# Kernel optimization log

Hardware: AMD Instinct MI355X
Metric: run time of the kernel (lower is better)

Reference implementation:

```python
import jax, jax.numpy as jnp
import numpy as np

N_NODES = 50000
N_EDGES = 640000
IN_CH = 32
OUT_CH = 64
H1 = 2 * IN_CH   # 64
H2 = 4 * IN_CH   # 128


def _sage_conv(x, src, dst, w_l, b_l, w_r, n_nodes):
    """PyG SAGEConv (mean aggr): out = mean_{j in N(i)} x_j @ w_l + b_l + x_i @ w_r."""
    msg = x[src]                                                  # [E, d] gather
    agg = jax.ops.segment_sum(msg, dst, num_segments=n_nodes)    # [N, d]
    cnt = jax.ops.segment_sum(jnp.ones_like(dst, x.dtype), dst, num_segments=n_nodes)
    mean = agg / jnp.maximum(cnt, 1.0)[:, None]                   # empty neighborhoods -> 0
    return mean @ w_l + b_l + x @ w_r


def setup_inputs() -> dict:
    key = jax.random.key(0)
    ks = jax.random.split(key, 9)
    x = jax.random.normal(ks[0], (N_NODES, IN_CH), dtype=jnp.float32)
    edge_index = jax.random.randint(ks[1], (2, N_EDGES), 0, N_NODES, dtype=jnp.int32)

    def glorot(k, shape):
        fan_in, fan_out = shape
        s = jnp.sqrt(6.0 / (fan_in + fan_out))
        return jax.random.uniform(k, shape, jnp.float32, -s, s)

    return {
        "x": x,
        "edge_index": edge_index,
        "w1_l": glorot(ks[2], (IN_CH, H1)), "b1": jnp.zeros((H1,), jnp.float32),
        "w1_r": glorot(ks[3], (IN_CH, H1)),
        "w2_l": glorot(ks[4], (H1, H2)), "b2": jnp.zeros((H2,), jnp.float32),
        "w2_r": glorot(ks[5], (H1, H2)),
        "w3_l": glorot(ks[6], (H2, OUT_CH)), "b3": jnp.zeros((OUT_CH,), jnp.float32),
        "w3_r": glorot(ks[7], (H2, OUT_CH)),
    }


def reference(x, edge_index, w1_l, b1, w1_r, w2_l, b2, w2_r, w3_l, b3, w3_r):
    n = x.shape[0]
    src, dst = edge_index[0], edge_index[1]
    h = jax.nn.relu(_sage_conv(x, src, dst, w1_l, b1, w1_r, n))
    h = jax.nn.relu(_sage_conv(h, src, dst, w2_l, b2, w2_r, n))
    return _sage_conv(h, src, dst, w3_l, b3, w3_r, n)
```

## Files before the change

### kernel.cpp

```cpp
#include <hip/hip_runtime.h>


typedef short bf8 __attribute__((ext_vector_type(8)));
typedef float f32x4 __attribute__((ext_vector_type(4)));

__device__ inline ushort bf16rn(float f) {
    unsigned u = __float_as_uint(f);
    return (ushort)((u + 0x7FFFu + ((u >> 16) & 1u)) >> 16);
}
__device__ inline float bf16tof(ushort h) {
    return __uint_as_float(((unsigned)h) << 16);
}
__device__ inline void split8(const float4 pa, const float4 pb, bf8& hi, bf8& lo) {
    const float v[8] = {pa.x, pa.y, pa.z, pa.w, pb.x, pb.y, pb.z, pb.w};
#pragma unroll
    for (int j = 0; j < 8; ++j) {
        const ushort h = bf16rn(v[j]);
        hi[j] = (short)h;
        lo[j] = (short)bf16rn(v[j] - bf16tof(h));
    }
}

__global__ __launch_bounds__(256) void prep_kernel(
    const float* __restrict__ x,
    const float* __restrict__ w1l, const float* __restrict__ w1r,
    const float* __restrict__ w2l, const float* __restrict__ w2r,
    const float* __restrict__ w3l, const float* __restrict__ w3r,
    ushort* __restrict__ wprep, int* __restrict__ cnt,
    ushort* __restrict__ xh, int nN, int nCntZero)
{
    const int g = blockIdx.x * 256 + threadIdx.x;
    const int n = gridDim.x * 256;
    for (int f = g; f < 9216; f += n) {
        int base, KCs, oc0, d0, wstride;
        const float *wa, *wb;
        if (f < 1024)      { base = 0;    KCs = 2; oc0 = 0;  wa = w1l; wb = w1r; d0 = 32;  wstride = 64;  }
        else if (f < 3072) { base = 1024; KCs = 4; oc0 = 0;  wa = w2l; wb = w2r; d0 = 64;  wstride = 128; }
        else if (f < 5120) { base = 3072; KCs = 4; oc0 = 64; wa = w2l; wb = w2r; d0 = 64;  wstride = 128; }
        else if (f < 7168) { base = 5120; KCs = 4; oc0 = 0;  wa = w3l; wb = w3l; d0 = 128; wstride = 64;  }
        else               { base = 7168; KCs = 4; oc0 = 0;  wa = w3r; wb = w3r; d0 = 128; wstride = 64;  }
        const int local = f - base;
        const int lane = local & 63;
        const int s = (local >> 6) & 1;
        const int kcct = local >> 7;
        const int kc = kcct % KCs;
        const int ct = kcct / KCs;
        const int col = oc0 + ct * 16 + (lane & 15);
        const int k0 = kc * 32 + (lane >> 4) * 8;
        ushort h8[8];
#pragma unroll
        for (int j = 0; j < 8; ++j) {
            const int k = k0 + j;
            const float* wr = (k < d0) ? (wa + (size_t)k * wstride)
                                       : (wb + (size_t)(k - d0) * wstride);
            const float v = wr[col];
            const ushort h = bf16rn(v);
            h8[j] = (s == 0) ? h : bf16rn(v - bf16tof(h));
        }
        *reinterpret_cast<int4*>(wprep + (size_t)f * 8) = *reinterpret_cast<const int4*>(h8);
    }
    for (int i = g; i < nCntZero / 4; i += n)
        reinterpret_cast<int4*>(cnt)[i] = make_int4(0, 0, 0, 0);
    const int nxv = nN * 4;
    for (int i = g; i < nxv; i += n) {
        const float4 a = reinterpret_cast<const float4*>(x)[i * 2 + 0];
        const float4 b = reinterpret_cast<const float4*>(x)[i * 2 + 1];
        const float v[8] = {a.x, a.y, a.z, a.w, b.x, b.y, b.z, b.w};
        bf8 h;
#pragma unroll
        for (int j = 0; j < 8; ++j) h[j] = (short)bf16rn(v[j]);
        reinterpret_cast<bf8*>(xh)[i] = h;
    }
}

__global__ __launch_bounds__(256) void count_kernel(const int* __restrict__ dst,
                                                    int* __restrict__ cnt,
                                                    ushort* __restrict__ pos, int nE) {
    int i = blockIdx.x * blockDim.x + threadIdx.x;
    int e0 = i * 4;
    if (e0 + 3 < nE) {
        int4 d = *reinterpret_cast<const int4*>(dst + e0);
        ushort4 p;
        p.x = (ushort)atomicAdd(&cnt[d.x], 1);
        p.y = (ushort)atomicAdd(&cnt[d.y], 1);
        p.z = (ushort)atomicAdd(&cnt[d.z], 1);
        p.w = (ushort)atomicAdd(&cnt[d.w], 1);
        *reinterpret_cast<ushort4*>(pos + e0) = p;
    } else {
        for (int e = e0; e < nE; ++e) pos[e] = (ushort)atomicAdd(&cnt[dst[e]], 1);
    }
}

__global__ __launch_bounds__(256) void scan_blocks(const int* __restrict__ cnt,
                                                   int* __restrict__ rowptr,
                                                   int* __restrict__ partials, int nN) {
    __shared__ int wsum[4];
    const int t = threadIdx.x;
    const int lane = t & 63, wid = t >> 6;
    const int base = blockIdx.x * 1024 + t * 4;

    int4 v = make_int4(0, 0, 0, 0);
    if (base + 3 < nN) {
        v = *reinterpret_cast<const int4*>(cnt + base);
    } else {
        if (base + 0 < nN) v.x = cnt[base + 0];
        if (base + 1 < nN) v.y = cnt[base + 1];
        if (base + 2 < nN) v.z = cnt[base + 2];
        if (base + 3 < nN) v.w = cnt[base + 3];
    }
    const int s = v.x + v.y + v.z + v.w;

    int inc = s;
#pragma unroll
    for (int d = 1; d < 64; d <<= 1) {
        int u = __shfl_up(inc, d);
        if (lane >= d) inc += u;
    }
    if (lane == 63) wsum[wid] = inc;
    __syncthreads();
    int woff = 0;
#pragma unroll
    for (int w = 0; w < 4; ++w) woff += (w < wid) ? wsum[w] : 0;

    const int excl = woff + inc - s;
    int4 o;
    o.x = excl; o.y = excl + v.x; o.z = excl + v.x + v.y; o.w = excl + v.x + v.y + v.z;
    if (base + 3 < nN) {
        *reinterpret_cast<int4*>(rowptr + base) = o;
    } else {
        if (base + 0 < nN) rowptr[base + 0] = o.x;
        if (base + 1 < nN) rowptr[base + 1] = o.y;
        if (base + 2 < nN) rowptr[base + 2] = o.z;
        if (base + 3 < nN) rowptr[base + 3] = o.w;
    }
    if (t == 255) partials[blockIdx.x] = woff + inc;
}

__global__ __launch_bounds__(256) void scan_add(int* __restrict__ rowptr,
                                                const int* __restrict__ partials,
                                                int nN, int nE) {
    __shared__ int soff;
    const int t = threadIdx.x;
    if (t < 64) {
        int v = (t < blockIdx.x) ? partials[t] : 0;
#pragma unroll
        for (int d = 32; d >= 1; d >>= 1) v += __shfl_xor(v, d);
        if (t == 0) soff = v;
    }
    __syncthreads();
    const int off = soff;
    const int base = blockIdx.x * 1024 + t * 4;
    if (base + 3 < nN) {
        int4 v = *reinterpret_cast<int4*>(rowptr + base);
        v.x += off; v.y += off; v.z += off; v.w += off;
        *reinterpret_cast<int4*>(rowptr + base) = v;
    } else {
        if (base + 0 < nN) rowptr[base + 0] += off;
        if (base + 1 < nN) rowptr[base + 1] += off;
        if (base + 2 < nN) rowptr[base + 2] += off;
        if (base + 3 < nN) rowptr[base + 3] += off;
    }
    if (blockIdx.x == 0 && t == 0) rowptr[nN] = nE;
}

__global__ __launch_bounds__(256) void fill_kernel(const int* __restrict__ src,
                                                   const int* __restrict__ dst,
                                                   const ushort* __restrict__ pos,
                                                   const int* __restrict__ rowptr,
                                                   ushort* __restrict__ csr_src, int nE) {
    int i = blockIdx.x * blockDim.x + threadIdx.x;
    int e0 = i * 4;
    if (e0 + 3 < nE) {
        int4 s4 = *reinterpret_cast<const int4*>(src + e0);
        int4 d4 = *reinterpret_cast<const int4*>(dst + e0);
        ushort4 p4 = *reinterpret_cast<const ushort4*>(pos + e0);
        csr_src[rowptr[d4.x] + p4.x] = (ushort)s4.x;
        csr_src[rowptr[d4.y] + p4.y] = (ushort)s4.y;
        csr_src[rowptr[d4.z] + p4.z] = (ushort)s4.z;
        csr_src[rowptr[d4.w] + p4.w] = (ushort)s4.w;
    } else {
        for (int e = e0; e < nE; ++e)
            csr_src[rowptr[dst[e]] + pos[e]] = (ushort)src[e];
    }
}

__global__ __launch_bounds__(256) void fused_layer1(
    const float* __restrict__ x, const ushort* __restrict__ xh,
    const int* __restrict__ rowptr, const ushort* __restrict__ csr_src,
    const ushort* __restrict__ wfrag, const float* __restrict__ b1,
    ushort* __restrict__ h1h, ushort* __restrict__ h1l, int nN)
{
    __shared__ float tile[64 * 36];
    __shared__ ushort wlds[1024 * 8];

    const int tid = threadIdx.x;
    const int node0 = blockIdx.x * 64;

    {
        const int4* wsrc = reinterpret_cast<const int4*>(wfrag);
        int4* wl = reinterpret_cast<int4*>(wlds);
        for (int i = tid; i < 1024; i += 256) wl[i] = wsrc[i];
    }
    {
        const int nl = tid >> 2;
        const int c = tid & 3;
        const int node = node0 + nl;
        float acc[8] = {0.f, 0.f, 0.f, 0.f, 0.f, 0.f, 0.f, 0.f};
        if (node < nN) {
            const int beg = rowptr[node], end = rowptr[node + 1];
            int e = beg;
            for (; e + 7 < end; e += 8) {
                int si[8];
#pragma unroll
                for (int j = 0; j < 8; ++j) si[j] = csr_src[e + j];
                bf8 v[8];
#pragma unroll
                for (int j = 0; j < 8; ++j)
                    v[j] = *reinterpret_cast<const bf8*>(xh + (size_t)si[j] * 32 + c * 8);
#pragma unroll
                for (int k = 0; k < 8; ++k)
#pragma unroll
                    for (int j = 0; j < 8; ++j) acc[k] += bf16tof((ushort)v[j][k]);
            }
            for (; e < end; ++e) {
                bf8 v = *reinterpret_cast<const bf8*>(xh + (size_t)csr_src[e] * 32 + c * 8);
#pragma unroll
                for (int k = 0; k < 8; ++k) acc[k] += bf16tof((ushort)v[k]);
            }
            const float sc = 1.0f / (float)max(end - beg, 1);
#pragma unroll
            for (int k = 0; k < 8; ++k) acc[k] *= sc;
        }
        *reinterpret_cast<float4*>(&tile[nl * 36 + c * 8 + 0]) =
            make_float4(acc[0], acc[1], acc[2], acc[3]);
        *reinterpret_cast<float4*>(&tile[nl * 36 + c * 8 + 4]) =
            make_float4(acc[4], acc[5], acc[6], acc[7]);
    }
    __syncthreads();

    const int w = tid >> 6, lane = tid & 63;
    const int rloc = w * 16 + (lane & 15);
    const int arow = min(node0 + rloc, nN - 1);
    const int kg = lane >> 4;
    bf8 ahi[2], alo[2];
    {
        const float* tp = &tile[rloc * 36 + kg * 8];
        split8(*reinterpret_cast<const float4*>(tp),
               *reinterpret_cast<const float4*>(tp + 4), ahi[0], alo[0]);
    }
    {
        const float* rp = x + (size_t)arow * 32 + kg * 8;
        split8(*reinterpret_cast<const float4*>(rp),
               *reinterpret_cast<const float4*>(rp + 4), ahi[1], alo[1]);
    }
    const bf8* bgl = reinterpret_cast<const bf8*>(wlds);
#pragma unroll
    for (int ct = 0; ct < 4; ++ct) {
        f32x4 acc = {0.f, 0.f, 0.f, 0.f};
#pragma unroll
        for (int kc = 0; kc < 2; ++kc) {
            const bf8 bhi = bgl[((ct * 2 + kc) * 2 + 0) * 64 + lane];
            const bf8 blo = bgl[((ct * 2 + kc) * 2 + 1) * 64 + lane];
            acc = __builtin_amdgcn_mfma_f32_16x16x32_bf16(ahi[kc], bhi, acc, 0, 0, 0);
            acc = __builtin_amdgcn_mfma_f32_16x16x32_bf16(ahi[kc], blo, acc, 0, 0, 0);
            acc = __builtin_amdgcn_mfma_f32_16x16x32_bf16(alo[kc], bhi, acc, 0, 0, 0);
        }
        const int col = ct * 16 + (lane & 15);
        const float bv = b1[col];
#pragma unroll
        for (int r = 0; r < 4; ++r) {
            const int node = node0 + w * 16 + (lane >> 4) * 4 + r;
            if (node < nN) {
                const float o = fmaxf(acc[r] + bv, 0.f);
                const ushort hi = bf16rn(o);
                h1h[(size_t)node * 64 + col] = hi;
                h1l[(size_t)node * 64 + col] = bf16rn(o - bf16tof(hi));
            }
        }
    }
}

__global__ __launch_bounds__(256) void fused_layer2(
    const ushort* __restrict__ h1h, const ushort* __restrict__ h1l,
    const int* __restrict__ rowptr, const ushort* __restrict__ csr_src,
    const ushort* __restrict__ wfrag, const float* __restrict__ b2,
    ushort* __restrict__ h2h, ushort* __restrict__ h2l, int nN)
{
    __shared__ float tile[64 * 68];

    const int tid = threadIdx.x;
    const int node0 = blockIdx.x * 64;

    {
        const int c = tid & 7;
        const int nl0 = tid >> 3;
#pragma unroll
        for (int p = 0; p < 2; ++p) {
            const int nl = p * 32 + nl0;
            const int node = node0 + nl;
            float acc[8] = {0.f, 0.f, 0.f, 0.f, 0.f, 0.f, 0.f, 0.f};
            if (node < nN) {
                const int beg = rowptr[node], end = rowptr[node + 1];
                int e = beg;
                for (; e + 7 < end; e += 8) {
                    int si[8];
#pragma unroll
                    for (int j = 0; j < 8; ++j) si[j] = csr_src[e + j];
                    bf8 v[8];
#pragma unroll
                    for (int j = 0; j < 8; ++j)
                        v[j] = *reinterpret_cast<const bf8*>(h1h + (size_t)si[j] * 64 + c * 8);
#pragma unroll
                    for (int k = 0; k < 8; ++k)
#pragma unroll
                        for (int j = 0; j < 8; ++j) acc[k] += bf16tof((ushort)v[j][k]);
                }
                for (; e < end; ++e) {
                    bf8 v = *reinterpret_cast<const bf8*>(h1h + (size_t)csr_src[e] * 64 + c * 8);
#pragma unroll
                    for (int k = 0; k < 8; ++k) acc[k] += bf16tof((ushort)v[k]);
                }
                const float sc = 1.0f / (float)max(end - beg, 1);
#pragma unroll
                for (int k = 0; k < 8; ++k) acc[k] *= sc;
            }
            *reinterpret_cast<float4*>(&tile[nl * 68 + c * 8 + 0]) =
                make_float4(acc[0], acc[1], acc[2], acc[3]);
            *reinterpret_cast<float4*>(&tile[nl * 68 + c * 8 + 4]) =
                make_float4(acc[4], acc[5], acc[6], acc[7]);
        }
    }
    __syncthreads();

    const int w = tid >> 6, lane = tid & 63;
    const int rloc = w * 16 + (lane & 15);
    const int arow = min(node0 + rloc, nN - 1);
    const int kg = lane >> 4;
    bf8 ahi[4], alo[4];
#pragma unroll
    for (int kc = 0; kc < 2; ++kc) {
        const float* tp = &tile[rloc * 68 + kc * 32 + kg * 8];
        split8(*reinterpret_cast<const float4*>(tp),
               *reinterpret_cast<const float4*>(tp + 4), ahi[kc], alo[kc]);
    }
#pragma unroll
    for (int kc = 2; kc < 4; ++kc) {
        const size_t off = (size_t)arow * 64 + (kc - 2) * 32 + kg * 8;
        ahi[kc] = *reinterpret_cast<const bf8*>(h1h + off);
        alo[kc] = *reinterpret_cast<const bf8*>(h1l + off);
    }
#pragma unroll
    for (int ct = 0; ct < 8; ++ct) {
        const int sec = ct >> 2, ctl = ct & 3;
        const bf8* bgl = reinterpret_cast<const bf8*>(wfrag) + sec * 2048;
        f32x4 acc = {0.f, 0.f, 0.f, 0.f};
#pragma unroll
        for (int kc = 0; kc < 4; ++kc) {
            const bf8 bhi = bgl[((ctl * 4 + kc) * 2 + 0) * 64 + lane];
            const bf8 blo = bgl[((ctl * 4 + kc) * 2 + 1) * 64 + lane];
            acc = __builtin_amdgcn_mfma_f32_16x16x32_bf16(ahi[kc], bhi, acc, 0, 0, 0);
            acc = __builtin_amdgcn_mfma_f32_16x16x32_bf16(ahi[kc], blo, acc, 0, 0, 0);
            acc = __builtin_amdgcn_mfma_f32_16x16x32_bf16(alo[kc], bhi, acc, 0, 0, 0);
        }
        const int col = ct * 16 + (lane & 15);
        const float bv = b2[col];
#pragma unroll
        for (int r = 0; r < 4; ++r) {
            const int node = node0 + w * 16 + (lane >> 4) * 4 + r;
            if (node < nN) {
                const float o = fmaxf(acc[r] + bv, 0.f);
                const ushort hi = bf16rn(o);
                h2h[(size_t)node * 128 + col] = hi;
                h2l[(size_t)node * 128 + col] = bf16rn(o - bf16tof(hi));
            }
        }
    }
}

__global__ __launch_bounds__(256) void mfma_dual(
    const ushort* __restrict__ h2h, const ushort* __restrict__ h2l,
    const ushort* __restrict__ wfrag, const float* __restrict__ b3,
    ushort* __restrict__ t3h, float* __restrict__ r3, int nN)
{
    const int tid = threadIdx.x;
    const int w = tid >> 6, lane = tid & 63;
    const int node0 = blockIdx.x * 64;
    const int arow = min(node0 + w * 16 + (lane & 15), nN - 1);
    const int kg = lane >> 4;

    bf8 ahi[4], alo[4];
#pragma unroll
    for (int kc = 0; kc < 4; ++kc) {
        const size_t off = (size_t)arow * 128 + kc * 32 + kg * 8;
        ahi[kc] = *reinterpret_cast<const bf8*>(h2h + off);
        alo[kc] = *reinterpret_cast<const bf8*>(h2l + off);
    }
#pragma unroll
    for (int sel = 0; sel < 2; ++sel) {
        const bf8* bgl = reinterpret_cast<const bf8*>(wfrag) + sel * 2048;
#pragma unroll
        for (int ct = 0; ct < 4; ++ct) {
            f32x4 acc = {0.f, 0.f, 0.f, 0.f};
#pragma unroll
            for (int kc = 0; kc < 4; ++kc) {
                const bf8 bhi = bgl[((ct * 4 + kc) * 2 + 0) * 64 + lane];
                const bf8 blo = bgl[((ct * 4 + kc) * 2 + 1) * 64 + lane];
                acc = __builtin_amdgcn_mfma_f32_16x16x32_bf16(ahi[kc], bhi, acc, 0, 0, 0);
                acc = __builtin_amdgcn_mfma_f32_16x16x32_bf16(ahi[kc], blo, acc, 0, 0, 0);
                acc = __builtin_amdgcn_mfma_f32_16x16x32_bf16(alo[kc], bhi, acc, 0, 0, 0);
            }
            const int col = ct * 16 + (lane & 15);
#pragma unroll
            for (int r = 0; r < 4; ++r) {
                const int node = node0 + w * 16 + (lane >> 4) * 4 + r;
                if (node < nN) {
                    if (sel) r3[(size_t)node * 64 + col] = acc[r] + b3[col];
                    else     t3h[(size_t)node * 64 + col] = bf16rn(acc[r]);
                }
            }
        }
    }
}

__global__ __launch_bounds__(256) void final_gather(
    const ushort* __restrict__ t3h, const int* __restrict__ rowptr,
    const ushort* __restrict__ csr_src, const float* __restrict__ r3,
    float* __restrict__ dout, int nN)
{
    const int tid = threadIdx.x;
    const int node = blockIdx.x * 32 + (tid >> 3);
    const int c = tid & 7;
    if (node >= nN) return;
    const int beg = rowptr[node], end = rowptr[node + 1];
    float acc[8] = {0.f, 0.f, 0.f, 0.f, 0.f, 0.f, 0.f, 0.f};
    int e = beg;
    for (; e + 7 < end; e += 8) {
        int si[8];
#pragma unroll
        for (int j = 0; j < 8; ++j) si[j] = csr_src[e + j];
        bf8 v[8];
#pragma unroll
        for (int j = 0; j < 8; ++j)
            v[j] = *reinterpret_cast<const bf8*>(t3h + (size_t)si[j] * 64 + c * 8);
#pragma unroll
        for (int k = 0; k < 8; ++k)
#pragma unroll
            for (int j = 0; j < 8; ++j) acc[k] += bf16tof((ushort)v[j][k]);
    }
    for (; e < end; ++e) {
        bf8 v = *reinterpret_cast<const bf8*>(t3h + (size_t)csr_src[e] * 64 + c * 8);
#pragma unroll
        for (int k = 0; k < 8; ++k) acc[k] += bf16tof((ushort)v[k]);
    }
    const float sc = 1.0f / (float)max(end - beg, 1);
    const float4 a0 = reinterpret_cast<const float4*>(r3)[(size_t)node * 16 + c * 2 + 0];
    const float4 a1 = reinterpret_cast<const float4*>(r3)[(size_t)node * 16 + c * 2 + 1];
    float4 o0, o1;
    o0.x = fmaf(acc[0], sc, a0.x); o0.y = fmaf(acc[1], sc, a0.y);
    o0.z = fmaf(acc[2], sc, a0.z); o0.w = fmaf(acc[3], sc, a0.w);
    o1.x = fmaf(acc[4], sc, a1.x); o1.y = fmaf(acc[5], sc, a1.y);
    o1.z = fmaf(acc[6], sc, a1.z); o1.w = fmaf(acc[7], sc, a1.w);
    reinterpret_cast<float4*>(dout)[(size_t)node * 16 + c * 2 + 0] = o0;
    reinterpret_cast<float4*>(dout)[(size_t)node * 16 + c * 2 + 1] = o1;
}

extern "C" void kernel_launch(void* const* d_in, const int* in_sizes, int n_in,
                              void* d_out, int out_size, void* d_ws, size_t ws_size,
                              hipStream_t stream) {
    const float* x   = (const float*)d_in[0];
    const int*   ei  = (const int*)d_in[1];
    const float* w1l = (const float*)d_in[2];
    const float* b1  = (const float*)d_in[3];
    const float* w1r = (const float*)d_in[4];
    const float* w2l = (const float*)d_in[5];
    const float* b2  = (const float*)d_in[6];
    const float* w2r = (const float*)d_in[7];
    const float* w3l = (const float*)d_in[8];
    const float* b3  = (const float*)d_in[9];
    const float* w3r = (const float*)d_in[10];

    const int nN = in_sizes[0] / 32;
    const int nE = in_sizes[1] / 2;
    const int* src = ei;
    const int* dst = ei + nE;
    const int nB = (nN + 1023) / 1024;
    const int nCntZero = (nN + 63) & ~63;

    char* ws = (char*)d_ws;
    size_t o = 0;
    auto alloc = [&](size_t nbytes) {
        char* p = ws + o;
        o += (nbytes + 255) & ~(size_t)255;
        return p;
    };
    int*    cnt      = (int*)alloc((size_t)nCntZero * sizeof(int));
    ushort* pos      = (ushort*)alloc((size_t)nE * sizeof(ushort));
    int*    partials = (int*)alloc(64 * sizeof(int));
    int*    rowptr   = (int*)alloc(((size_t)nN + 1) * sizeof(int));
    ushort* csr_src  = (ushort*)alloc((size_t)nE * sizeof(ushort));
    ushort* wprep    = (ushort*)alloc((size_t)9216 * 8 * sizeof(ushort));
    ushort* xh       = (ushort*)alloc((size_t)nN * 32 * sizeof(ushort));
    ushort* h1h      = (ushort*)alloc((size_t)nN * 64 * sizeof(ushort));
    ushort* h1l      = (ushort*)alloc((size_t)nN * 64 * sizeof(ushort));
    ushort* h2h      = (ushort*)alloc((size_t)nN * 128 * sizeof(ushort));
    ushort* h2l      = (ushort*)alloc((size_t)nN * 128 * sizeof(ushort));
    ushort* t3h      = (ushort*)alloc((size_t)nN * 64 * sizeof(ushort));
    float*  r3       = (float*)alloc((size_t)nN * 64 * sizeof(float));

    prep_kernel<<<784, 256, 0, stream>>>(x, w1l, w1r, w2l, w2r, w3l, w3r,
                                         wprep, cnt, xh, nN, nCntZero);
    count_kernel<<<(nE / 4 + 255) / 256, 256, 0, stream>>>(dst, cnt, pos, nE);
    scan_blocks<<<nB, 256, 0, stream>>>(cnt, rowptr, partials, nN);
    scan_add<<<nB, 256, 0, stream>>>(rowptr, partials, nN, nE);
    fill_kernel<<<(nE / 4 + 255) / 256, 256, 0, stream>>>(src, dst, pos, rowptr, csr_src, nE);

    const int xblk = (nN + 63) / 64;

    fused_layer1<<<xblk, 256, 0, stream>>>(x, xh, rowptr, csr_src, wprep, b1, h1h, h1l, nN);
    fused_layer2<<<xblk, 256, 0, stream>>>(h1h, h1l, rowptr, csr_src,
                                           wprep + (size_t)1024 * 8, b2, h2h, h2l, nN);
    mfma_dual<<<xblk, 256, 0, stream>>>(h2h, h2l, wprep + (size_t)5120 * 8, b3, t3h, r3, nN);
    final_gather<<<(nN + 31) / 32, 256, 0, stream>>>(t3h, rowptr, csr_src, r3, (float*)d_out, nN);
}
```

Before: 141.1 us.

## Halve node tile in fused layers, split MFMA columns across waves, store r3 as bf16

Layers 1 and 2 now handle 32 nodes per 256-thread block instead of 64. Each gathering thread covers a narrower feature slice (4 channels in layer 1), and in the MFMA phase the four waves split into two row groups and two column groups. Layer 1 reads weight fragments directly from global memory instead of staging them in LDS. Together this doubles the block count and cuts per-thread serial gather work. Separately, the layer-3 root term r3 is stored as bf16 instead of fp32, halving that intermediate's traffic at the cost of some output precision.

```diff
diff --git a/kernel.cpp b/kernel.cpp
--- a/kernel.cpp
+++ b/kernel.cpp
@@ -2,6 +2,7 @@
 
 
 typedef short bf8 __attribute__((ext_vector_type(8)));
+typedef short bf4 __attribute__((ext_vector_type(4)));
 typedef float f32x4 __attribute__((ext_vector_type(4)));
 
 __device__ inline ushort bf16rn(float f) {
@@ -190,20 +191,104 @@
     const ushort* __restrict__ wfrag, const float* __restrict__ b1,
     ushort* __restrict__ h1h, ushort* __restrict__ h1l, int nN)
 {
-    __shared__ float tile[64 * 36];
-    __shared__ ushort wlds[1024 * 8];
+    __shared__ float tile[32 * 36];
 
     const int tid = threadIdx.x;
-    const int node0 = blockIdx.x * 64;
+    const int node0 = blockIdx.x * 32;
 
     {
-        const int4* wsrc = reinterpret_cast<const int4*>(wfrag);
-        int4* wl = reinterpret_cast<int4*>(wlds);
-        for (int i = tid; i < 1024; i += 256) wl[i] = wsrc[i];
-    }
+        const int nl = tid >> 3;
+        const int c = tid & 7;
+        const int node = node0 + nl;
+        float acc[4] = {0.f, 0.f, 0.f, 0.f};
+        if (node < nN) {
+            const int beg = rowptr[node], end = rowptr[node + 1];
+            int e = beg;
+            for (; e + 7 < end; e += 8) {
+                int si[8];
+#pragma unroll
+                for (int j = 0; j < 8; ++j) si[j] = csr_src[e + j];
+                bf4 v[8];
+#pragma unroll
+                for (int j = 0; j < 8; ++j)
+                    v[j] = *reinterpret_cast<const bf4*>(xh + (size_t)si[j] * 32 + c * 4);
+#pragma unroll
+                for (int k = 0; k < 4; ++k)
+#pragma unroll
+                    for (int j = 0; j < 8; ++j) acc[k] += bf16tof((ushort)v[j][k]);
+            }
+            for (; e < end; ++e) {
+                bf4 v = *reinterpret_cast<const bf4*>(xh + (size_t)csr_src[e] * 32 + c * 4);
+#pragma unroll
+                for (int k = 0; k < 4; ++k) acc[k] += bf16tof((ushort)v[k]);
+            }
+            const float sc = 1.0f / (float)max(end - beg, 1);
+#pragma unroll
+            for (int k = 0; k < 4; ++k) acc[k] *= sc;
+        }
+        *reinterpret_cast<float4*>(&tile[nl * 36 + c * 4]) =
+            make_float4(acc[0], acc[1], acc[2], acc[3]);
+    }
+    __syncthreads();
+
+    const int w = tid >> 6, lane = tid & 63;
+    const int rg = w & 1, cg = w >> 1;
+    const int rloc = rg * 16 + (lane & 15);
+    const int arow = min(node0 + rloc, nN - 1);
+    const int kg = lane >> 4;
+    bf8 ahi[2], alo[2];
     {
-        const int nl = tid >> 2;
-        const int c = tid & 3;
+        const float* tp = &tile[rloc * 36 + kg * 8];
+        split8(*reinterpret_cast<const float4*>(tp),
+               *reinterpret_cast<const float4*>(tp + 4), ahi[0], alo[0]);
+    }
+    {
+        const float* rp = x + (size_t)arow * 32 + kg * 8;
+        split8(*reinterpret_cast<const float4*>(rp),
+               *reinterpret_cast<const float4*>(rp + 4), ahi[1], alo[1]);
+    }
+    const bf8* bgl = reinterpret_cast<const bf8*>(wfrag);
+#pragma unroll
+    for (int cc = 0; cc < 2; ++cc) {
+        const int ct = cg * 2 + cc;
+        f32x4 acc = {0.f, 0.f, 0.f, 0.f};
+#pragma unroll
+        for (int kc = 0; kc < 2; ++kc) {
+            const bf8 bhi = bgl[((ct * 2 + kc) * 2 + 0) * 64 + lane];
+            const bf8 blo = bgl[((ct * 2 + kc) * 2 + 1) * 64 + lane];
+            acc = __builtin_amdgcn_mfma_f32_16x16x32_bf16(ahi[kc], bhi, acc, 0, 0, 0);
+            acc = __builtin_amdgcn_mfma_f32_16x16x32_bf16(ahi[kc], blo, acc, 0, 0, 0);
+            acc = __builtin_amdgcn_mfma_f32_16x16x32_bf16(alo[kc], bhi, acc, 0, 0, 0);
+        }
+        const int col = ct * 16 + (lane & 15);
+        const float bv = b1[col];
+#pragma unroll
+        for (int r = 0; r < 4; ++r) {
+            const int node = node0 + rg * 16 + (lane >> 4) * 4 + r;
+            if (node < nN) {
+                const float o = fmaxf(acc[r] + bv, 0.f);
+                const ushort hi = bf16rn(o);
+                h1h[(size_t)node * 64 + col] = hi;
+                h1l[(size_t)node * 64 + col] = bf16rn(o - bf16tof(hi));
+            }
+        }
+    }
+}
+
+__global__ __launch_bounds__(256) void fused_layer2(
+    const ushort* __restrict__ h1h, const ushort* __restrict__ h1l,
+    const int* __restrict__ rowptr, const ushort* __restrict__ csr_src,
+    const ushort* __restrict__ wfrag, const float* __restrict__ b2,
+    ushort* __restrict__ h2h, ushort* __restrict__ h2l, int nN)
+{
+    __shared__ float tile[32 * 68];
+
+    const int tid = threadIdx.x;
+    const int node0 = blockIdx.x * 32;
+
+    {
+        const int nl = tid >> 3;
+        const int c = tid & 7;
         const int node = node0 + nl;
         float acc[8] = {0.f, 0.f, 0.f, 0.f, 0.f, 0.f, 0.f, 0.f};
         if (node < nN) {
@@ -216,14 +301,14 @@
                 bf8 v[8];
 #pragma unroll
                 for (int j = 0; j < 8; ++j)
-                    v[j] = *reinterpret_cast<const bf8*>(xh + (size_t)si[j] * 32 + c * 8);
+                    v[j] = *reinterpret_cast<const bf8*>(h1h + (size_t)si[j] * 64 + c * 8);
 #pragma unroll
                 for (int k = 0; k < 8; ++k)
 #pragma unroll
                     for (int j = 0; j < 8; ++j) acc[k] += bf16tof((ushort)v[j][k]);
             }
             for (; e < end; ++e) {
-                bf8 v = *reinterpret_cast<const bf8*>(xh + (size_t)csr_src[e] * 32 + c * 8);
+                bf8 v = *reinterpret_cast<const bf8*>(h1h + (size_t)csr_src[e] * 64 + c * 8);
 #pragma unroll
                 for (int k = 0; k < 8; ++k) acc[k] += bf16tof((ushort)v[k]);
             }
@@ -231,109 +316,16 @@
 #pragma unroll
             for (int k = 0; k < 8; ++k) acc[k] *= sc;
         }
-        *reinterpret_cast<float4*>(&tile[nl * 36 + c * 8 + 0]) =
+        *reinterpret_cast<float4*>(&tile[nl * 68 + c * 8 + 0]) =
             make_float4(acc[0], acc[1], acc[2], acc[3]);
-        *reinterpret_cast<float4*>(&tile[nl * 36 + c * 8 + 4]) =
+        *reinterpret_cast<float4*>(&tile[nl * 68 + c * 8 + 4]) =
             make_float4(acc[4], acc[5], acc[6], acc[7]);
     }
     __syncthreads();
 
     const int w = tid >> 6, lane = tid & 63;
-    const int rloc = w * 16 + (lane & 15);
-    const int arow = min(node0 + rloc, nN - 1);
-    const int kg = lane >> 4;
-    bf8 ahi[2], alo[2];
-    {
-        const float* tp = &tile[rloc * 36 + kg * 8];
-        split8(*reinterpret_cast<const float4*>(tp),
-               *reinterpret_cast<const float4*>(tp + 4), ahi[0], alo[0]);
-    }
-    {
-        const float* rp = x + (size_t)arow * 32 + kg * 8;
-        split8(*reinterpret_cast<const float4*>(rp),
-               *reinterpret_cast<const float4*>(rp + 4), ahi[1], alo[1]);
-    }
-    const bf8* bgl = reinterpret_cast<const bf8*>(wlds);
-#pragma unroll
-    for (int ct = 0; ct < 4; ++ct) {
-        f32x4 acc = {0.f, 0.f, 0.f, 0.f};
-#pragma unroll
-        for (int kc = 0; kc < 2; ++kc) {
-            const bf8 bhi = bgl[((ct * 2 + kc) * 2 + 0) * 64 + lane];
-            const bf8 blo = bgl[((ct * 2 + kc) * 2 + 1) * 64 + lane];
-            acc = __builtin_amdgcn_mfma_f32_16x16x32_bf16(ahi[kc], bhi, acc, 0, 0, 0);
-            acc = __builtin_amdgcn_mfma_f32_16x16x32_bf16(ahi[kc], blo, acc, 0, 0, 0);
-            acc = __builtin_amdgcn_mfma_f32_16x16x32_bf16(alo[kc], bhi, acc, 0, 0, 0);
-        }
-        const int col = ct * 16 + (lane & 15);
-        const float bv = b1[col];
-#pragma unroll
-        for (int r = 0; r < 4; ++r) {
-            const int node = node0 + w * 16 + (lane >> 4) * 4 + r;
-            if (node < nN) {
-                const float o = fmaxf(acc[r] + bv, 0.f);
-                const ushort hi = bf16rn(o);
-                h1h[(size_t)node * 64 + col] = hi;
-                h1l[(size_t)node * 64 + col] = bf16rn(o - bf16tof(hi));
-            }
-        }
-    }
-}
-
-__global__ __launch_bounds__(256) void fused_layer2(
-    const ushort* __restrict__ h1h, const ushort* __restrict__ h1l,
-    const int* __restrict__ rowptr, const ushort* __restrict__ csr_src,
-    const ushort* __restrict__ wfrag, const float* __restrict__ b2,
-    ushort* __restrict__ h2h, ushort* __restrict__ h2l, int nN)
-{
-    __shared__ float tile[64 * 68];
-
-    const int tid = threadIdx.x;
-    const int node0 = blockIdx.x * 64;
-
-    {
-        const int c = tid & 7;
-        const int nl0 = tid >> 3;
-#pragma unroll
-        for (int p = 0; p < 2; ++p) {
-            const int nl = p * 32 + nl0;
-            const int node = node0 + nl;
-            float acc[8] = {0.f, 0.f, 0.f, 0.f, 0.f, 0.f, 0.f, 0.f};
-            if (node < nN) {
-                const int beg = rowptr[node], end = rowptr[node + 1];
-                int e = beg;
-                for (; e + 7 < end; e += 8) {
-                    int si[8];
-#pragma unroll
-                    for (int j = 0; j < 8; ++j) si[j] = csr_src[e + j];
-                    bf8 v[8];
-#pragma unroll
-                    for (int j = 0; j < 8; ++j)
-                        v[j] = *reinterpret_cast<const bf8*>(h1h + (size_t)si[j] * 64 + c * 8);
-#pragma unroll
-                    for (int k = 0; k < 8; ++k)
-#pragma unroll
-                        for (int j = 0; j < 8; ++j) acc[k] += bf16tof((ushort)v[j][k]);
-                }
-                for (; e < end; ++e) {
-                    bf8 v = *reinterpret_cast<const bf8*>(h1h + (size_t)csr_src[e] * 64 + c * 8);
-#pragma unroll
-                    for (int k = 0; k < 8; ++k) acc[k] += bf16tof((ushort)v[k]);
-                }
-                const float sc = 1.0f / (float)max(end - beg, 1);
-#pragma unroll
-                for (int k = 0; k < 8; ++k) acc[k] *= sc;
-            }
-            *reinterpret_cast<float4*>(&tile[nl * 68 + c * 8 + 0]) =
-                make_float4(acc[0], acc[1], acc[2], acc[3]);
-            *reinterpret_cast<float4*>(&tile[nl * 68 + c * 8 + 4]) =
-                make_float4(acc[4], acc[5], acc[6], acc[7]);
-        }
-    }
-    __syncthreads();
-
-    const int w = tid >> 6, lane = tid & 63;
-    const int rloc = w * 16 + (lane & 15);
+    const int rg = w & 1, cg = w >> 1;
+    const int rloc = rg * 16 + (lane & 15);
     const int arow = min(node0 + rloc, nN - 1);
     const int kg = lane >> 4;
     bf8 ahi[4], alo[4];
@@ -349,10 +341,9 @@
         ahi[kc] = *reinterpret_cast<const bf8*>(h1h + off);
         alo[kc] = *reinterpret_cast<const bf8*>(h1l + off);
     }
-#pragma unroll
-    for (int ct = 0; ct < 8; ++ct) {
-        const int sec = ct >> 2, ctl = ct & 3;
-        const bf8* bgl = reinterpret_cast<const bf8*>(wfrag) + sec * 2048;
+    const bf8* bgl = reinterpret_cast<const bf8*>(wfrag) + cg * 2048;
+#pragma unroll
+    for (int ctl = 0; ctl < 4; ++ctl) {
         f32x4 acc = {0.f, 0.f, 0.f, 0.f};
 #pragma unroll
         for (int kc = 0; kc < 4; ++kc) {
@@ -362,11 +353,11 @@
             acc = __builtin_amdgcn_mfma_f32_16x16x32_bf16(ahi[kc], blo, acc, 0, 0, 0);
             acc = __builtin_amdgcn_mfma_f32_16x16x32_bf16(alo[kc], bhi, acc, 0, 0, 0);
         }
-        const int col = ct * 16 + (lane & 15);
+        const int col = cg * 64 + ctl * 16 + (lane & 15);
         const float bv = b2[col];
 #pragma unroll
         for (int r = 0; r < 4; ++r) {
-            const int node = node0 + w * 16 + (lane >> 4) * 4 + r;
+            const int node = node0 + rg * 16 + (lane >> 4) * 4 + r;
             if (node < nN) {
                 const float o = fmaxf(acc[r] + bv, 0.f);
                 const ushort hi = bf16rn(o);
@@ -380,7 +371,7 @@
 __global__ __launch_bounds__(256) void mfma_dual(
     const ushort* __restrict__ h2h, const ushort* __restrict__ h2l,
     const ushort* __restrict__ wfrag, const float* __restrict__ b3,
-    ushort* __restrict__ t3h, float* __restrict__ r3, int nN)
+    ushort* __restrict__ t3h, ushort* __restrict__ r3h, int nN)
 {
     const int tid = threadIdx.x;
     const int w = tid >> 6, lane = tid & 63;
@@ -414,7 +405,7 @@
             for (int r = 0; r < 4; ++r) {
                 const int node = node0 + w * 16 + (lane >> 4) * 4 + r;
                 if (node < nN) {
-                    if (sel) r3[(size_t)node * 64 + col] = acc[r] + b3[col];
+                    if (sel) r3h[(size_t)node * 64 + col] = bf16rn(acc[r] + b3[col]);
                     else     t3h[(size_t)node * 64 + col] = bf16rn(acc[r]);
                 }
             }
@@ -424,7 +415,7 @@
 
 __global__ __launch_bounds__(256) void final_gather(
     const ushort* __restrict__ t3h, const int* __restrict__ rowptr,
-    const ushort* __restrict__ csr_src, const float* __restrict__ r3,
+    const ushort* __restrict__ csr_src, const ushort* __restrict__ r3h,
     float* __restrict__ dout, int nN)
 {
     const int tid = threadIdx.x;
@@ -453,13 +444,16 @@
         for (int k = 0; k < 8; ++k) acc[k] += bf16tof((ushort)v[k]);
     }
     const float sc = 1.0f / (float)max(end - beg, 1);
-    const float4 a0 = reinterpret_cast<const float4*>(r3)[(size_t)node * 16 + c * 2 + 0];
-    const float4 a1 = reinterpret_cast<const float4*>(r3)[(size_t)node * 16 + c * 2 + 1];
+    const bf8 a = *reinterpret_cast<const bf8*>(r3h + (size_t)node * 64 + c * 8);
     float4 o0, o1;
-    o0.x = fmaf(acc[0], sc, a0.x); o0.y = fmaf(acc[1], sc, a0.y);
-    o0.z = fmaf(acc[2], sc, a0.z); o0.w = fmaf(acc[3], sc, a0.w);
-    o1.x = fmaf(acc[4], sc, a1.x); o1.y = fmaf(acc[5], sc, a1.y);
-    o1.z = fmaf(acc[6], sc, a1.z); o1.w = fmaf(acc[7], sc, a1.w);
+    o0.x = fmaf(acc[0], sc, bf16tof((ushort)a[0]));
+    o0.y = fmaf(acc[1], sc, bf16tof((ushort)a[1]));
+    o0.z = fmaf(acc[2], sc, bf16tof((ushort)a[2]));
+    o0.w = fmaf(acc[3], sc, bf16tof((ushort)a[3]));
+    o1.x = fmaf(acc[4], sc, bf16tof((ushort)a[4]));
+    o1.y = fmaf(acc[5], sc, bf16tof((ushort)a[5]));
+    o1.z = fmaf(acc[6], sc, bf16tof((ushort)a[6]));
+    o1.w = fmaf(acc[7], sc, bf16tof((ushort)a[7]));
     reinterpret_cast<float4*>(dout)[(size_t)node * 16 + c * 2 + 0] = o0;
     reinterpret_cast<float4*>(dout)[(size_t)node * 16 + c * 2 + 1] = o1;
 }
@@ -505,7 +499,7 @@
     ushort* h2h      = (ushort*)alloc((size_t)nN * 128 * sizeof(ushort));
     ushort* h2l      = (ushort*)alloc((size_t)nN * 128 * sizeof(ushort));
     ushort* t3h      = (ushort*)alloc((size_t)nN * 64 * sizeof(ushort));
-    float*  r3       = (float*)alloc((size_t)nN * 64 * sizeof(float));
+    ushort* r3h      = (ushort*)alloc((size_t)nN * 64 * sizeof(ushort));
 
     prep_kernel<<<784, 256, 0, stream>>>(x, w1l, w1r, w2l, w2r, w3l, w3r,
                                          wprep, cnt, xh, nN, nCntZero);
@@ -514,11 +508,12 @@
     scan_add<<<nB, 256, 0, stream>>>(rowptr, partials, nN, nE);
     fill_kernel<<<(nE / 4 + 255) / 256, 256, 0, stream>>>(src, dst, pos, rowptr, csr_src, nE);
 
-    const int xblk = (nN + 63) / 64;
-
-    fused_layer1<<<xblk, 256, 0, stream>>>(x, xh, rowptr, csr_src, wprep, b1, h1h, h1l, nN);
-    fused_layer2<<<xblk, 256, 0, stream>>>(h1h, h1l, rowptr, csr_src,
-                                           wprep + (size_t)1024 * 8, b2, h2h, h2l, nN);
-    mfma_dual<<<xblk, 256, 0, stream>>>(h2h, h2l, wprep + (size_t)5120 * 8, b3, t3h, r3, nN);
-    final_gather<<<(nN + 31) / 32, 256, 0, stream>>>(t3h, rowptr, csr_src, r3, (float*)d_out, nN);
-}
+    const int xblk32 = (nN + 31) / 32;
+    const int xblk64 = (nN + 63) / 64;
+
+    fused_layer1<<<xblk32, 256, 0, stream>>>(x, xh, rowptr, csr_src, wprep, b1, h1h, h1l, nN);
+    fused_layer2<<<xblk32, 256, 0, stream>>>(h1h, h1l, rowptr, csr_src,
+                                             wprep + (size_t)1024 * 8, b2, h2h, h2l, nN);
+    mfma_dual<<<xblk64, 256, 0, stream>>>(h2h, h2l, wprep + (size_t)5120 * 8, b3, t3h, r3h, nN);
+    final_gather<<<(nN + 31) / 32, 256, 0, stream>>>(t3h, rowptr, csr_src, r3h, (float*)d_out, nN);
+}
```

Measured after the change: 141.7 us. About the same (+0.4%).
